# Kernel optimization log

Measured on AMD Instinct MI355X. Metric: run time of the kernel, lower is better.

The kernel has to match this reference:

```python
import jax, jax.numpy as jnp
import numpy as np

B, R, C, H = 2048, 100, 64, 256  # batch graphs, regions/graph, in_channels, hidden
N = B * R                         # total nodes
E = 3276800                       # edges


def setup_inputs() -> dict:
    key = jax.random.key(0)
    ks = jax.random.split(key, 12)
    state = jax.random.normal(ks[0], (N, C), dtype=jnp.float32)
    edge_index = jax.random.randint(ks[1], (2, E), 0, N, dtype=jnp.int64)
    action = jax.random.uniform(ks[2], (B, R, R), dtype=jnp.float32)
    s = lambda f: 1.0 / np.sqrt(f)
    W_gcn = jax.random.uniform(ks[3], (C, C), jnp.float32, -s(C), s(C))
    b_gcn = jnp.zeros((C,), jnp.float32)
    W1 = jax.random.uniform(ks[4], (C + R, H), jnp.float32, -s(C + R), s(C + R))
    b1 = jax.random.uniform(ks[5], (H,), jnp.float32, -s(C + R), s(C + R))
    W2 = jax.random.uniform(ks[6], (H, H), jnp.float32, -s(H), s(H))
    b2 = jax.random.uniform(ks[7], (H,), jnp.float32, -s(H), s(H))
    W3 = jax.random.uniform(ks[8], (H, 1), jnp.float32, -s(H), s(H))
    b3 = jax.random.uniform(ks[9], (1,), jnp.float32, -s(H), s(H))
    return {"state": state, "edge_index": edge_index, "action": action,
            "W_gcn": W_gcn, "b_gcn": b_gcn, "W1": W1, "b1": b1,
            "W2": W2, "b2": b2, "W3": W3, "b3": b3}


def gcn_conv(x, edge_index, W, b):
    # PyG GCNConv: add self-loops, symmetric degree normalization, then aggregate.
    n = x.shape[0]
    loops = jnp.arange(n, dtype=edge_index.dtype)
    src = jnp.concatenate([edge_index[0], loops])
    dst = jnp.concatenate([edge_index[1], loops])
    deg = jax.ops.segment_sum(jnp.ones_like(dst, dtype=x.dtype), dst, num_segments=n)
    dinv = deg ** -0.5  # deg >= 1 thanks to self-loops
    xw = x @ W
    msg = xw[src] * (dinv[src] * dinv[dst])[:, None]
    return jax.ops.segment_sum(msg, dst, num_segments=n) + b


def reference(state, edge_index, action, W_gcn, b_gcn, W1, b1, W2, b2, W3, b3):
    out = jax.nn.relu(gcn_conv(state, edge_index, W_gcn, b_gcn))
    x = out + state                              # residual, [N, C]
    x = x.reshape(-1, R, C)                      # [B, R, C]
    concat = jnp.concatenate([x, action], axis=-1)  # [B, R, C+R]
    x = jax.nn.relu(concat @ W1 + b1)
    x = jax.nn.relu(x @ W2 + b2)
    x = jnp.sum(x, axis=1)                       # sum pooling over regions -> [B, H]
    return (x @ W3 + b3).squeeze(-1)             # [B]
```

## Files before the change

### kernel.cpp

```cpp
#include <hip/hip_runtime.h>
#include <hip/hip_bf16.h>
#include <cstdint>
#include <cstddef>

#define N_NODES 204800
#define N_EDGES 3276800
#define NB 2048
#define NR 100
#define NC 64
#define NH 256
#define KPAD 192
#define NBKT 400
#define H1P 264

typedef __attribute__((ext_vector_type(8))) short short8;
typedef __attribute__((ext_vector_type(4))) float f32x4;
typedef unsigned int uint32;

__device__ __forceinline__ void gload16(const void* g, void* l) {
    __builtin_amdgcn_global_load_lds(
        (const __attribute__((address_space(1))) uint32_t*)(g),
        (__attribute__((address_space(3))) uint32_t*)(l), 16, 0, 0);
}

__device__ __forceinline__ ushort f2bf(float v) {
    __hip_bfloat16 h = __float2bfloat16(v);
    return *reinterpret_cast<ushort*>(&h);
}

__device__ __forceinline__ uint32 pack2bf(float a, float b) {
    return (uint32)f2bf(a) | ((uint32)f2bf(b) << 16);
}

__device__ __forceinline__ float bflo(uint32 v) { return __uint_as_float(v << 16); }
__device__ __forceinline__ float bfhi(uint32 v) { return __uint_as_float(v & 0xFFFF0000u); }


__global__ __launch_bounds__(256) void k_bhist(const int* __restrict__ ei,
                                               int* __restrict__ bcnt) {
    __shared__ int h[NBKT];
    int t = threadIdx.x;
    for (int i = t; i < NBKT; i += 256) h[i] = 0;
    __syncthreads();
    #pragma unroll 8
    for (int k = 0; k < 8; ++k) {
        int e = blockIdx.x * 2048 + k * 256 + t;
        atomicAdd(&h[ei[N_EDGES + e] >> 9], 1);
    }
    __syncthreads();
    for (int i = t; i < NBKT; i += 256)
        if (h[i]) atomicAdd(&bcnt[i], h[i]);
}

__global__ void k_bscan(const int* __restrict__ bcnt, int* __restrict__ boffs,
                        int* __restrict__ bcur) {
    __shared__ int tmp[512];
    int t = threadIdx.x;
    int v = (t < NBKT) ? bcnt[t] : 0;
    tmp[t] = v;
    __syncthreads();
    for (int off = 1; off < 512; off <<= 1) {
        int x = 0;
        if (t >= off) x = tmp[t - off];
        __syncthreads();
        tmp[t] += x;
        __syncthreads();
    }
    if (t < NBKT) {
        int o = tmp[t] - v;
        boffs[t] = o;
        bcur[t] = o;
    }
}

__global__ __launch_bounds__(256) void k_bscat(const int* __restrict__ ei,
                                               int* __restrict__ bcur,
                                               uint32* __restrict__ part) {
    __shared__ int hist[NBKT];
    int tid = threadIdx.x;
    for (int i = tid; i < NBKT; i += 256) hist[i] = 0;
    __syncthreads();

    uint32 w[8];
    int bk[8], r[8];
    #pragma unroll 8
    for (int k = 0; k < 8; ++k) {
        int e = blockIdx.x * 2048 + k * 256 + tid;
        int s = ei[e];
        int d = ei[N_EDGES + e];
        int b = d >> 9;
        w[k] = (uint32)s | ((uint32)(d & 511) << 18);
        bk[k] = b;
        r[k] = atomicAdd(&hist[b], 1);
    }
    __syncthreads();
    for (int i = tid; i < NBKT; i += 256) {
        int c = hist[i];
        hist[i] = c ? atomicAdd(&bcur[i], c) : 0;
    }
    __syncthreads();
    #pragma unroll 8
    for (int k = 0; k < 8; ++k)
        part[hist[bk[k]] + r[k]] = w[k];
}

__global__ __launch_bounds__(512) void k_sortb(
    const uint32* __restrict__ part, const int* __restrict__ boffs,
    const int* __restrict__ bcnt, int* __restrict__ csr,
    int* __restrict__ cnt, int* __restrict__ offs, float* __restrict__ dinv) {
    __shared__ int h[512];
    __shared__ int cur[512];
    int b = blockIdx.x, t = threadIdx.x;
    h[t] = 0;
    __syncthreads();
    int base = boffs[b], n = bcnt[b];
    for (int i = t; i < n; i += 512)
        atomicAdd(&h[part[base + i] >> 18], 1);
    __syncthreads();
    int v = h[t];
    int node = b * 512 + t;
    cnt[node] = v;
    dinv[node] = rsqrtf((float)(v + 1));
    __syncthreads();
    for (int off = 1; off < 512; off <<= 1) {
        int x = 0;
        if (t >= off) x = h[t - off];
        __syncthreads();
        h[t] += x;
        __syncthreads();
    }
    int excl = h[t] - v;
    offs[node] = base + excl;
    cur[t] = excl;
    __syncthreads();
    for (int i = t; i < n; i += 512) {
        uint32 ew = part[base + i];
        int dl = ew >> 18;
        int pos = atomicAdd(&cur[dl], 1);
        csr[base + pos] = (int)(ew & 0x3FFFF);
    }
}

__global__ void k_ssb(const float* __restrict__ state, const float* __restrict__ dinv,
                      uint32* __restrict__ ssb32) {
    int idx = blockIdx.x * 256 + threadIdx.x;
    int row = idx >> 5;
    float d = dinv[row];
    float2 v = reinterpret_cast<const float2*>(state)[idx];
    ssb32[idx] = pack2bf(v.x * d, v.y * d);
}

__global__ __launch_bounds__(256) void k_gcn(
    const uint32* __restrict__ ssb32, const float* __restrict__ state,
    const int* __restrict__ csr, const int* __restrict__ offs,
    const int* __restrict__ cnt, const float* __restrict__ dinv,
    const ushort* __restrict__ Wgt, const float* __restrict__ bg,
    ushort* __restrict__ xb16) {
    __shared__ uint32 av[32 * 36];
    __shared__ ushort wgs[64 * 72];
    int tid = threadIdx.x;
    int w = tid >> 6, lane = tid & 63;
    int half = lane >> 5, l = lane & 31;
    int R0 = blockIdx.x * 32;

    {
        int r = tid >> 2, c0 = (tid & 3) * 16;
        short8 v0 = *(const short8*)(Wgt + r * 64 + c0);
        short8 v1 = *(const short8*)(Wgt + r * 64 + c0 + 8);
        *(short8*)(wgs + r * 72 + c0) = v0;
        *(short8*)(wgs + r * 72 + c0 + 8) = v1;
    }

    for (int rr = 0; rr < 4; ++rr) {
        int lrow = w * 8 + rr * 2 + half;
        int row = R0 + lrow;
        float di = dinv[row];
        float2 st2 = *reinterpret_cast<const float2*>(state + (size_t)row * 64 + 2 * l);
        int s0 = offs[row], c = cnt[row];
        float x0 = 0.f, y0 = 0.f, x1 = 0.f, y1 = 0.f;
        float x2 = 0.f, y2 = 0.f, x3 = 0.f, y3 = 0.f;
        int e = 0;
        for (; e + 8 <= c; e += 8) {
            int sa = csr[s0 + e + 0];
            int sb = csr[s0 + e + 1];
            int sc = csr[s0 + e + 2];
            int sd = csr[s0 + e + 3];
            int se = csr[s0 + e + 4];
            int sf = csr[s0 + e + 5];
            int sg = csr[s0 + e + 6];
            int sh = csr[s0 + e + 7];
            uint32 va = ssb32[(size_t)sa * 32 + l];
            uint32 vb = ssb32[(size_t)sb * 32 + l];
            uint32 vc = ssb32[(size_t)sc * 32 + l];
            uint32 vd = ssb32[(size_t)sd * 32 + l];
            uint32 ve = ssb32[(size_t)se * 32 + l];
            uint32 vf = ssb32[(size_t)sf * 32 + l];
            uint32 vg = ssb32[(size_t)sg * 32 + l];
            uint32 vh = ssb32[(size_t)sh * 32 + l];
            x0 += bflo(va); y0 += bfhi(va);
            x1 += bflo(vb); y1 += bfhi(vb);
            x2 += bflo(vc); y2 += bfhi(vc);
            x3 += bflo(vd); y3 += bfhi(vd);
            x0 += bflo(ve); y0 += bfhi(ve);
            x1 += bflo(vf); y1 += bfhi(vf);
            x2 += bflo(vg); y2 += bfhi(vg);
            x3 += bflo(vh); y3 += bfhi(vh);
        }
        for (; e + 4 <= c; e += 4) {
            int sa = csr[s0 + e + 0];
            int sb = csr[s0 + e + 1];
            int sc = csr[s0 + e + 2];
            int sd = csr[s0 + e + 3];
            uint32 va = ssb32[(size_t)sa * 32 + l];
            uint32 vb = ssb32[(size_t)sb * 32 + l];
            uint32 vc = ssb32[(size_t)sc * 32 + l];
            uint32 vd = ssb32[(size_t)sd * 32 + l];
            x0 += bflo(va); y0 += bfhi(va);
            x1 += bflo(vb); y1 += bfhi(vb);
            x2 += bflo(vc); y2 += bfhi(vc);
            x3 += bflo(vd); y3 += bfhi(vd);
        }
        for (; e < c; ++e) {
            int s = csr[s0 + e];
            uint32 v = ssb32[(size_t)s * 32 + l];
            x0 += bflo(v); y0 += bfhi(v);
        }
        float ax = ((x0 + x1) + (x2 + x3)) * di + di * di * st2.x;
        float ay = ((y0 + y1) + (y2 + y3)) * di + di * di * st2.y;
        av[lrow * 36 + l] = pack2bf(ax, ay);
    }
    __syncthreads();

    int l15 = lane & 15, l4 = lane >> 4;
    const ushort* avs = (const ushort*)av;
    f32x4 acc[2] = {};
    #pragma unroll
    for (int kk = 0; kk < 2; ++kk) {
        short8 bf = *(const short8*)(wgs + (w * 16 + l15) * 72 + kk * 32 + l4 * 8);
        #pragma unroll
        for (int mt = 0; mt < 2; ++mt) {
            short8 af = *(const short8*)(avs + (mt * 16 + l15) * 72 + kk * 32 + l4 * 8);
            acc[mt] = __builtin_amdgcn_mfma_f32_16x16x32_bf16(af, bf, acc[mt], 0, 0, 0);
        }
    }
    int col = w * 16 + l15;
    float bgv = bg[col];
    #pragma unroll
    for (int mt = 0; mt < 2; ++mt)
        #pragma unroll
        for (int r = 0; r < 4; ++r) {
            int row = R0 + mt * 16 + l4 * 4 + r;
            float v = fmaxf(acc[mt][r] + bgv, 0.f) + state[(size_t)row * 64 + col];
            xb16[(size_t)row * 64 + col] = f2bf(v);
        }
}

__global__ void k_packW(const float* __restrict__ W1, const float* __restrict__ W2,
                        const float* __restrict__ Wg, ushort* __restrict__ W1t,
                        ushort* __restrict__ W2t, ushort* __restrict__ Wgt) {
    int t = blockIdx.x * 256 + threadIdx.x;
    if (t < 256 * KPAD) {
        int j = t / KPAD, k = t % KPAD;
        W1t[t] = (k < NC + NR) ? f2bf(W1[(size_t)k * NH + j]) : (ushort)0;
    } else if (t < 256 * KPAD + 256 * 256) {
        int t2 = t - 256 * KPAD;
        int j = t2 / 256, k = t2 % 256;
        W2t[t2] = f2bf(W2[(size_t)k * NH + j]);
    } else {
        int t3 = t - 256 * KPAD - 256 * 256;
        if (t3 < 64 * 64) {
            int n = t3 >> 6, k = t3 & 63;
            Wgt[t3] = f2bf(Wg[(size_t)k * 64 + n]);
        }
    }
}

__global__ __launch_bounds__(256, 3) void k_mlpf(
    const ushort* __restrict__ xb16, const float* __restrict__ action,
    const ushort* __restrict__ W1t, const ushort* __restrict__ W2t,
    const float* __restrict__ b1, const float* __restrict__ b2,
    const float* __restrict__ W3, float* __restrict__ out) {
    __shared__ __align__(16) ushort As[64 * 32];
    __shared__ __align__(16) ushort Bs[256 * 32];
    __shared__ __align__(16) ushort H1s[64 * H1P];
    int tid = threadIdx.x;
    int w = tid >> 6, lane = tid & 63;
    int m0 = blockIdx.x * 64;
    int l15 = lane & 15, l4 = lane >> 4;
    int arow = tid >> 2, aseg = tid & 3;

    int gr = m0 + arow;
    int gb = gr / 100, grr = gr - gb * 100;
    const float* abp = action + (size_t)gb * 10000 + (size_t)grr * 100;

    float b1v[4], b2v[4], w3v[4];
    #pragma unroll
    for (int nt = 0; nt < 4; ++nt) {
        int col = w * 64 + nt * 16 + l15;
        b1v[nt] = b1[col];
        b2v[nt] = b2[col];
        w3v[nt] = W3[col];
    }

    f32x4 acc[4][4] = {};

    for (int kt = 0; kt < 6; ++kt) {
        int k0 = kt * 32;
        if (kt < 2) {
            gload16(xb16 + (size_t)(m0 + arow) * 64 + k0 + aseg * 8,
                    (char*)As + tid * 16);
        } else {
            int col0 = (k0 - 64) + aseg * 8;
            ushort tmp[8];
            #pragma unroll
            for (int u = 0; u < 8; ++u) {
                int cc = col0 + u;
                tmp[u] = (cc < NR) ? f2bf(abp[cc]) : (ushort)0;
            }
            *(short8*)((char*)As + tid * 16) = *(const short8*)tmp;
        }
        #pragma unroll
        for (int i = 0; i < 4; ++i)
            gload16(W1t + (size_t)(i * 64 + arow) * KPAD + k0 + aseg * 8,
                    (char*)Bs + i * 4096 + tid * 16);
        __syncthreads();
        short8 af[4], bf[4];
        #pragma unroll
        for (int mt = 0; mt < 4; ++mt)
            af[mt] = *(const short8*)((const char*)As + (mt * 16 + l15) * 64 + l4 * 16);
        #pragma unroll
        for (int nt = 0; nt < 4; ++nt)
            bf[nt] = *(const short8*)((const char*)Bs + (w * 64 + nt * 16 + l15) * 64 + l4 * 16);
        #pragma unroll
        for (int mt = 0; mt < 4; ++mt)
            #pragma unroll
            for (int nt = 0; nt < 4; ++nt)
                acc[mt][nt] = __builtin_amdgcn_mfma_f32_16x16x32_bf16(
                    af[mt], bf[nt], acc[mt][nt], 0, 0, 0);
        __syncthreads();
    }

    #pragma unroll
    for (int mt = 0; mt < 4; ++mt)
        #pragma unroll
        for (int nt = 0; nt < 4; ++nt) {
            int col = w * 64 + nt * 16 + l15;
            #pragma unroll
            for (int r = 0; r < 4; ++r) {
                int row = mt * 16 + l4 * 4 + r;
                H1s[row * H1P + col] = f2bf(fmaxf(acc[mt][nt][r] + b1v[nt], 0.f));
            }
        }
    #pragma unroll
    for (int mt = 0; mt < 4; ++mt)
        #pragma unroll
        for (int nt = 0; nt < 4; ++nt)
            acc[mt][nt] = (f32x4){0.f, 0.f, 0.f, 0.f};
    __syncthreads();

    for (int kt = 0; kt < 8; ++kt) {
        int k0 = kt * 32;
        #pragma unroll
        for (int i = 0; i < 4; ++i)
            gload16(W2t + (size_t)(i * 64 + arow) * 256 + k0 + aseg * 8,
                    (char*)Bs + i * 4096 + tid * 16);
        __syncthreads();
        short8 af[4], bf[4];
        #pragma unroll
        for (int mt = 0; mt < 4; ++mt)
            af[mt] = *(const short8*)((const char*)H1s +
                     ((size_t)(mt * 16 + l15) * H1P + k0 + l4 * 8) * 2);
        #pragma unroll
        for (int nt = 0; nt < 4; ++nt)
            bf[nt] = *(const short8*)((const char*)Bs + (w * 64 + nt * 16 + l15) * 64 + l4 * 16);
        #pragma unroll
        for (int mt = 0; mt < 4; ++mt)
            #pragma unroll
            for (int nt = 0; nt < 4; ++nt)
                acc[mt][nt] = __builtin_amdgcn_mfma_f32_16x16x32_bf16(
                    af[mt], bf[nt], acc[mt][nt], 0, 0, 0);
        __syncthreads();
    }

    float* red = (float*)As;
    #pragma unroll
    for (int mt = 0; mt < 4; ++mt)
        #pragma unroll
        for (int r = 0; r < 4; ++r) {
            float v = 0.f;
            #pragma unroll
            for (int nt = 0; nt < 4; ++nt)
                v += fmaxf(acc[mt][nt][r] + b2v[nt], 0.f) * w3v[nt];
            v += __shfl_xor(v, 1);
            v += __shfl_xor(v, 2);
            v += __shfl_xor(v, 4);
            v += __shfl_xor(v, 8);
            if (l15 == 0) red[(mt * 16 + l4 * 4 + r) * 4 + w] = v;
        }
    __syncthreads();
    if (tid < 64) {
        float s = red[tid * 4 + 0] + red[tid * 4 + 1] + red[tid * 4 + 2] + red[tid * 4 + 3];
        int gbase = m0;
        int g0 = gbase / 100;
        int r0 = gbase - g0 * 100;
        int split = 100 - r0; if (split > 64) split = 64;
        float v0 = (tid < split) ? s : 0.f;
        float vs = s;
        #pragma unroll
        for (int d = 1; d < 64; d <<= 1) {
            v0 += __shfl_xor(v0, d);
            vs += __shfl_xor(vs, d);
        }
        if (tid == 0) {
            atomicAdd(&out[g0], v0);
            if (split < 64) atomicAdd(&out[g0 + 1], vs - v0);
        }
    }
}

__global__ void k_init_out(float* __restrict__ out, const float* __restrict__ b3) {
    int i = blockIdx.x * 256 + threadIdx.x;
    out[i] = b3[0];
}


extern "C" void kernel_launch(void* const* d_in, const int* in_sizes, int n_in,
                              void* d_out, int out_size, void* d_ws, size_t ws_size,
                              hipStream_t stream) {
    const float* state  = (const float*)d_in[0];
    const int*   ei     = (const int*)d_in[1];
    const float* action = (const float*)d_in[2];
    const float* Wg     = (const float*)d_in[3];
    const float* bg     = (const float*)d_in[4];
    const float* W1     = (const float*)d_in[5];
    const float* b1     = (const float*)d_in[6];
    const float* W2     = (const float*)d_in[7];
    const float* b2     = (const float*)d_in[8];
    const float* W3     = (const float*)d_in[9];
    const float* b3     = (const float*)d_in[10];
    float* out = (float*)d_out;

    char* ws = (char*)d_ws;
    uint32* part  = (uint32*)(ws + 0);
    uint32* ssb32 = (uint32*)(ws + 13107200);
    ushort* xb16  = (ushort*)(ws + 39321600);
    int*   csr    = (int*)  (ws + 65536000);
    int*   cnt    = (int*)  (ws + 78643200);
    int*   offs   = (int*)  (ws + 79462400);
    float* dinv   = (float*)(ws + 80281600);
    int*   bcnt   = (int*)  (ws + 81100800);
    int*   boffs  = (int*)  (ws + 81102400);
    int*   bcur   = (int*)  (ws + 81104000);
    ushort* W1t   = (ushort*)(ws + 81105600);
    ushort* W2t   = (ushort*)(ws + 81203904);
    ushort* Wgt   = (ushort*)(ws + 81334976);

    hipMemsetAsync(bcnt, 0, NBKT * sizeof(int), stream);
    k_init_out<<<NB / 256, 256, 0, stream>>>(out, b3);

    k_bhist<<<N_EDGES / 2048, 256, 0, stream>>>(ei, bcnt);
    k_bscan<<<1, 512, 0, stream>>>(bcnt, boffs, bcur);
    k_bscat<<<N_EDGES / 2048, 256, 0, stream>>>(ei, bcur, part);
    k_sortb<<<NBKT, 512, 0, stream>>>(part, boffs, bcnt, csr, cnt, offs, dinv);
    k_ssb<<<(N_NODES * 32) / 256, 256, 0, stream>>>(state, dinv, ssb32);
    k_packW<<<(256 * KPAD + 256 * 256 + 64 * 64 + 255) / 256, 256, 0, stream>>>(
        W1, W2, Wg, W1t, W2t, Wgt);
    k_gcn<<<N_NODES / 32, 256, 0, stream>>>(ssb32, state, csr, offs, cnt, dinv,
                                            Wgt, bg, xb16);
    k_mlpf<<<N_NODES / 64, 256, 0, stream>>>(xb16, action, W1t, W2t, b1, b2, W3, out);
}
```

Before: 332.1 us.

## Double-buffer MLP GEMM tiles and pre-swizzle weights into fragment order

```diff
diff --git a/kernel.cpp b/kernel.cpp
--- a/kernel.cpp
+++ b/kernel.cpp
@@ -256,18 +256,28 @@
 }
 
 __global__ void k_packW(const float* __restrict__ W1, const float* __restrict__ W2,
-                        const float* __restrict__ Wg, ushort* __restrict__ W1t,
-                        ushort* __restrict__ W2t, ushort* __restrict__ Wgt) {
+                        const float* __restrict__ Wg, ushort* __restrict__ W1f,
+                        ushort* __restrict__ W2f, ushort* __restrict__ Wgt) {
     int t = blockIdx.x * 256 + threadIdx.x;
-    if (t < 256 * KPAD) {
-        int j = t / KPAD, k = t % KPAD;
-        W1t[t] = (k < NC + NR) ? f2bf(W1[(size_t)k * NH + j]) : (ushort)0;
-    } else if (t < 256 * KPAD + 256 * 256) {
-        int t2 = t - 256 * KPAD;
-        int j = t2 / 256, k = t2 % 256;
-        W2t[t2] = f2bf(W2[(size_t)k * NH + j]);
+    if (t < 6 * 4 * 256 * 8) {
+        int u = t & 7, chunk = t >> 3;
+        int tid = chunk & 255, ktI = chunk >> 8;
+        int kt = ktI >> 2, i = ktI & 3;
+        int l = tid & 63, wp = tid >> 6;
+        int k = kt * 32 + (l >> 4) * 8 + u;
+        int j = i * 64 + wp * 16 + (l & 15);
+        W1f[t] = (k < NC + NR) ? f2bf(W1[(size_t)k * NH + j]) : (ushort)0;
+    } else if (t < 49152 + 8 * 4 * 256 * 8) {
+        int t2 = t - 49152;
+        int u = t2 & 7, chunk = t2 >> 3;
+        int tid = chunk & 255, ktI = chunk >> 8;
+        int kt = ktI >> 2, i = ktI & 3;
+        int l = tid & 63, wp = tid >> 6;
+        int k = kt * 32 + (l >> 4) * 8 + u;
+        int j = i * 64 + wp * 16 + (l & 15);
+        W2f[t2] = f2bf(W2[(size_t)k * NH + j]);
     } else {
-        int t3 = t - 256 * KPAD - 256 * 256;
+        int t3 = t - 49152 - 65536;
         if (t3 < 64 * 64) {
             int n = t3 >> 6, k = t3 & 63;
             Wgt[t3] = f2bf(Wg[(size_t)k * 64 + n]);
@@ -275,20 +285,21 @@
     }
 }
 
-__global__ __launch_bounds__(256, 3) void k_mlpf(
+__global__ __launch_bounds__(256, 2) void k_mlpf(
     const ushort* __restrict__ xb16, const float* __restrict__ action,
-    const ushort* __restrict__ W1t, const ushort* __restrict__ W2t,
+    const ushort* __restrict__ W1f, const ushort* __restrict__ W2f,
     const float* __restrict__ b1, const float* __restrict__ b2,
     const float* __restrict__ W3, float* __restrict__ out) {
-    __shared__ __align__(16) ushort As[64 * 32];
-    __shared__ __align__(16) ushort Bs[256 * 32];
+    __shared__ __align__(16) ushort As[2][64 * 32];
+    __shared__ __align__(16) ushort Bs[2][256 * 32];
     __shared__ __align__(16) ushort H1s[64 * H1P];
     int tid = threadIdx.x;
     int w = tid >> 6, lane = tid & 63;
     int m0 = blockIdx.x * 64;
     int l15 = lane & 15, l4 = lane >> 4;
-    int arow = tid >> 2, aseg = tid & 3;
-
+
+    int arow = (tid >> 6) * 16 + (tid & 15);
+    int aseg = (tid >> 4) & 3;
     int gr = m0 + arow;
     int gb = gr / 100, grr = gr - gb * 100;
     const float* abp = action + (size_t)gb * 10000 + (size_t)grr * 100;
@@ -304,33 +315,92 @@
 
     f32x4 acc[4][4] = {};
 
+    #pragma unroll
+    for (int i = 0; i < 4; ++i)
+        gload16(W1f + ((size_t)(0 * 4 + i) * 256 + tid) * 8, (char*)Bs[0] + i * 4096 + tid * 16);
+    gload16(xb16 + (size_t)gr * 64 + 0 * 32 + aseg * 8, (char*)As[0] + tid * 16);
+    __syncthreads();
+
+    int cur = 0;
     for (int kt = 0; kt < 6; ++kt) {
+        int nxt = cur ^ 1;
+        if (kt < 5) {
+            #pragma unroll
+            for (int i = 0; i < 4; ++i)
+                gload16(W1f + ((size_t)((kt + 1) * 4 + i) * 256 + tid) * 8,
+                        (char*)Bs[nxt] + i * 4096 + tid * 16);
+            if (kt + 1 < 2) {
+                gload16(xb16 + (size_t)gr * 64 + (kt + 1) * 32 + aseg * 8,
+                        (char*)As[nxt] + tid * 16);
+            } else {
+                int c0 = (kt + 1) * 32 - 64 + aseg * 8;
+                ushort tmp[8];
+                #pragma unroll
+                for (int u = 0; u < 8; ++u) {
+                    int cc = c0 + u;
+                    tmp[u] = (cc < NR) ? f2bf(abp[cc]) : (ushort)0;
+                }
+                *(short8*)((char*)As[nxt] + tid * 16) = *(const short8*)tmp;
+            }
+        } else {
+            #pragma unroll
+            for (int i = 0; i < 4; ++i)
+                gload16(W2f + ((size_t)(0 * 4 + i) * 256 + tid) * 8,
+                        (char*)Bs[nxt] + i * 4096 + tid * 16);
+        }
+        short8 af[4], bf[4];
+        #pragma unroll
+        for (int mt = 0; mt < 4; ++mt)
+            af[mt] = *(const short8*)((const char*)As[cur] + mt * 1024 + lane * 16);
+        #pragma unroll
+        for (int nt = 0; nt < 4; ++nt)
+            bf[nt] = *(const short8*)((const char*)Bs[cur] + w * 4096 + nt * 1024 + lane * 16);
+        #pragma unroll
+        for (int mt = 0; mt < 4; ++mt)
+            #pragma unroll
+            for (int nt = 0; nt < 4; ++nt)
+                acc[mt][nt] = __builtin_amdgcn_mfma_f32_16x16x32_bf16(
+                    af[mt], bf[nt], acc[mt][nt], 0, 0, 0);
+        if (kt == 5) {
+            #pragma unroll
+            for (int mt = 0; mt < 4; ++mt)
+                #pragma unroll
+                for (int nt = 0; nt < 4; ++nt) {
+                    int col = w * 64 + nt * 16 + l15;
+                    #pragma unroll
+                    for (int r = 0; r < 4; ++r) {
+                        int row = mt * 16 + l4 * 4 + r;
+                        H1s[row * H1P + col] = f2bf(fmaxf(acc[mt][nt][r] + b1v[nt], 0.f));
+                    }
+                }
+        }
+        __syncthreads();
+        cur = nxt;
+    }
+
+    #pragma unroll
+    for (int mt = 0; mt < 4; ++mt)
+        #pragma unroll
+        for (int nt = 0; nt < 4; ++nt)
+            acc[mt][nt] = (f32x4){0.f, 0.f, 0.f, 0.f};
+
+    for (int kt = 0; kt < 8; ++kt) {
+        int nxt = cur ^ 1;
+        if (kt < 7) {
+            #pragma unroll
+            for (int i = 0; i < 4; ++i)
+                gload16(W2f + ((size_t)((kt + 1) * 4 + i) * 256 + tid) * 8,
+                        (char*)Bs[nxt] + i * 4096 + tid * 16);
+        }
         int k0 = kt * 32;
-        if (kt < 2) {
-            gload16(xb16 + (size_t)(m0 + arow) * 64 + k0 + aseg * 8,
-                    (char*)As + tid * 16);
-        } else {
-            int col0 = (k0 - 64) + aseg * 8;
-            ushort tmp[8];
-            #pragma unroll
-            for (int u = 0; u < 8; ++u) {
-                int cc = col0 + u;
-                tmp[u] = (cc < NR) ? f2bf(abp[cc]) : (ushort)0;
-            }
-            *(short8*)((char*)As + tid * 16) = *(const short8*)tmp;
-        }
-        #pragma unroll
-        for (int i = 0; i < 4; ++i)
-            gload16(W1t + (size_t)(i * 64 + arow) * KPAD + k0 + aseg * 8,
-                    (char*)Bs + i * 4096 + tid * 16);
-        __syncthreads();
         short8 af[4], bf[4];
         #pragma unroll
         for (int mt = 0; mt < 4; ++mt)
-            af[mt] = *(const short8*)((const char*)As + (mt * 16 + l15) * 64 + l4 * 16);
+            af[mt] = *(const short8*)((const char*)H1s +
+                     ((size_t)(mt * 16 + l15) * H1P + k0 + l4 * 8) * 2);
         #pragma unroll
         for (int nt = 0; nt < 4; ++nt)
-            bf[nt] = *(const short8*)((const char*)Bs + (w * 64 + nt * 16 + l15) * 64 + l4 * 16);
+            bf[nt] = *(const short8*)((const char*)Bs[cur] + w * 4096 + nt * 1024 + lane * 16);
         #pragma unroll
         for (int mt = 0; mt < 4; ++mt)
             #pragma unroll
@@ -338,48 +408,7 @@
                 acc[mt][nt] = __builtin_amdgcn_mfma_f32_16x16x32_bf16(
                     af[mt], bf[nt], acc[mt][nt], 0, 0, 0);
         __syncthreads();
-    }
-
-    #pragma unroll
-    for (int mt = 0; mt < 4; ++mt)
-        #pragma unroll
-        for (int nt = 0; nt < 4; ++nt) {
-            int col = w * 64 + nt * 16 + l15;
-            #pragma unroll
-            for (int r = 0; r < 4; ++r) {
-                int row = mt * 16 + l4 * 4 + r;
-                H1s[row * H1P + col] = f2bf(fmaxf(acc[mt][nt][r] + b1v[nt], 0.f));
-            }
-        }
-    #pragma unroll
-    for (int mt = 0; mt < 4; ++mt)
-        #pragma unroll
-        for (int nt = 0; nt < 4; ++nt)
-            acc[mt][nt] = (f32x4){0.f, 0.f, 0.f, 0.f};
-    __syncthreads();
-
-    for (int kt = 0; kt < 8; ++kt) {
-        int k0 = kt * 32;
-        #pragma unroll
-        for (int i = 0; i < 4; ++i)
-            gload16(W2t + (size_t)(i * 64 + arow) * 256 + k0 + aseg * 8,
-                    (char*)Bs + i * 4096 + tid * 16);
-        __syncthreads();
-        short8 af[4], bf[4];
-        #pragma unroll
-        for (int mt = 0; mt < 4; ++mt)
-            af[mt] = *(const short8*)((const char*)H1s +
-                     ((size_t)(mt * 16 + l15) * H1P + k0 + l4 * 8) * 2);
-        #pragma unroll
-        for (int nt = 0; nt < 4; ++nt)
-            bf[nt] = *(const short8*)((const char*)Bs + (w * 64 + nt * 16 + l15) * 64 + l4 * 16);
-        #pragma unroll
-        for (int mt = 0; mt < 4; ++mt)
-            #pragma unroll
-            for (int nt = 0; nt < 4; ++nt)
-                acc[mt][nt] = __builtin_amdgcn_mfma_f32_16x16x32_bf16(
-                    af[mt], bf[nt], acc[mt][nt], 0, 0, 0);
-        __syncthreads();
+        cur = nxt;
     }
 
     float* red = (float*)As;
@@ -451,8 +480,8 @@
     int*   bcnt   = (int*)  (ws + 81100800);
     int*   boffs  = (int*)  (ws + 81102400);
     int*   bcur   = (int*)  (ws + 81104000);
-    ushort* W1t   = (ushort*)(ws + 81105600);
-    ushort* W2t   = (ushort*)(ws + 81203904);
+    ushort* W1f   = (ushort*)(ws + 81105600);
+    ushort* W2f   = (ushort*)(ws + 81203904);
     ushort* Wgt   = (ushort*)(ws + 81334976);
 
     hipMemsetAsync(bcnt, 0, NBKT * sizeof(int), stream);
@@ -463,9 +492,9 @@
     k_bscat<<<N_EDGES / 2048, 256, 0, stream>>>(ei, bcur, part);
     k_sortb<<<NBKT, 512, 0, stream>>>(part, boffs, bcnt, csr, cnt, offs, dinv);
     k_ssb<<<(N_NODES * 32) / 256, 256, 0, stream>>>(state, dinv, ssb32);
-    k_packW<<<(256 * KPAD + 256 * 256 + 64 * 64 + 255) / 256, 256, 0, stream>>>(
-        W1, W2, Wg, W1t, W2t, Wgt);
+    k_packW<<<(49152 + 65536 + 4096 + 255) / 256, 256, 0, stream>>>(
+        W1, W2, Wg, W1f, W2f, Wgt);
     k_gcn<<<N_NODES / 32, 256, 0, stream>>>(ssb32, state, csr, offs, cnt, dinv,
                                             Wgt, bg, xb16);
-    k_mlpf<<<N_NODES / 64, 256, 0, stream>>>(xb16, action, W1t, W2t, b1, b2, W3, out);
-}
+    k_mlpf<<<N_NODES / 64, 256, 0, stream>>>(xb16, action, W1f, W2f, b1, b2, W3, out);
+}
```

Measured after the change: 324.7 us. 2.2% less time.
